# Optimization experiments

Hardware: AMD Instinct MI355X
Metric: run time of the kernel (lower is better)

The kernel has to match this reference:

```python
import jax, jax.numpy as jnp
import numpy as np

B, S, D = 2, 2048, 1024
H = 16
DK = D // H  # 64
THETA = 10000.0
CLAMP = 80.0


def setup_inputs() -> dict:
    key = jax.random.key(0)
    ks = jax.random.split(key, 5)
    scale = 1.0 / np.sqrt(D)
    return {
        "x": jax.random.normal(ks[0], (B, S, D), jnp.float32),
        "Wq": jax.random.normal(ks[1], (D, D), jnp.float32) * scale,
        "Wk": jax.random.normal(ks[2], (D, D), jnp.float32) * scale,
        "Wv": jax.random.normal(ks[3], (D, D), jnp.float32) * scale,
        "Wo": jax.random.normal(ks[4], (D, D), jnp.float32) * scale,
    }


def _rope(x):
    # x: (B, H, S, DK); rotate interleaved even/odd pairs
    pos = jnp.arange(S, dtype=jnp.float32)  # token_positions = arange
    inv_freq = 1.0 / (THETA ** (jnp.arange(0, DK, 2, dtype=jnp.float32) / DK))
    ang = pos[:, None] * inv_freq[None, :]  # (S, DK/2)
    cos, sin = jnp.cos(ang), jnp.sin(ang)
    x1, x2 = x[..., 0::2], x[..., 1::2]
    r1 = x1 * cos - x2 * sin
    r2 = x1 * sin + x2 * cos
    out = jnp.stack([r1, r2], axis=-1).reshape(x.shape)
    return out


def reference(x, Wq, Wk, Wv, Wo):
    # fused-style QKV projections (bias-free Linear: y = x @ W^T)
    def proj(W):
        y = jnp.einsum('bsd,ed->bse', x, W)
        return y.reshape(B, S, H, DK).transpose(0, 2, 1, 3)  # b h s dk
    Q, K, V = proj(Wq), proj(Wk), proj(Wv)
    Q, K = _rope(Q), _rope(K)
    # naive attention with score clamp then causal mask then scaled softmax
    scores = jnp.einsum('bhqd,bhkd->bhqk', Q, K)
    scores = jnp.clip(scores, -CLAMP, CLAMP)
    causal = jnp.tril(jnp.ones((S, S), dtype=bool))  # (q, k)
    scores = jnp.where(causal, scores, -jnp.inf)
    weights = jax.nn.softmax(scores / np.sqrt(DK), axis=-1)
    att = jnp.einsum('bhqk,bhkd->bhqd', weights, V)
    att = att.transpose(0, 2, 1, 3).reshape(B, S, D)
    return jnp.einsum('bsd,ed->bse', att, Wo)
```

## Files before the change

kernel.cpp:

```cpp
#include <hip/hip_runtime.h>
#include <hip/hip_bf16.h>

#define Bc 2
#define Sc 2048
#define Dc 1024
#define Hc 16
#define DKc 64
#define Mrows 4096

typedef __bf16 bf16;
typedef __bf16 bf16x8 __attribute__((ext_vector_type(8)));
typedef __bf16 bf16x4 __attribute__((ext_vector_type(4)));
typedef float f32x4 __attribute__((ext_vector_type(4)));

__global__ void cvt_f32_bf16(const float* __restrict__ in, bf16* __restrict__ out, int n) {
    int idx = (blockIdx.x * blockDim.x + threadIdx.x) * 4;
    if (idx < n) {
        float4 v = *(const float4*)(in + idx);
        bf16x4 o = { (bf16)v.x, (bf16)v.y, (bf16)v.z, (bf16)v.w };
        *(bf16x4*)(out + idx) = o;
    }
}

__global__ void cvt_w4(const float* __restrict__ a, const float* __restrict__ b,
                       const float* __restrict__ c, const float* __restrict__ d,
                       bf16* __restrict__ oa, bf16* __restrict__ ob,
                       bf16* __restrict__ oc, bf16* __restrict__ od) {
    int idx = (blockIdx.x * blockDim.x + threadIdx.x) * 4;
    const float* in; bf16* out;
    switch (blockIdx.y) {
        case 0: in = a; out = oa; break;
        case 1: in = b; out = ob; break;
        case 2: in = c; out = oc; break;
        default: in = d; out = od; break;
    }
    float4 v = *(const float4*)(in + idx);
    bf16x4 o = { (bf16)v.x, (bf16)v.y, (bf16)v.z, (bf16)v.w };
    *(bf16x4*)(out + idx) = o;
}

__device__ __forceinline__ void gld_lds16(const bf16* g, bf16* l) {
    __builtin_amdgcn_global_load_lds((const __attribute__((address_space(1))) void*)g,
                                     (__attribute__((address_space(3))) void*)l, 16, 0, 0);
}

template <typename OutT>
__global__ __launch_bounds__(512) void gemm_bt(const bf16* __restrict__ A,
                                               const bf16* __restrict__ Bt,
                                               OutT* __restrict__ C,
                                               int M, int N, int K) {
    __shared__ bf16 As[128 * 64];
    __shared__ bf16 Bs[128 * 64];
    const int tid = threadIdx.x;
    const int bm = blockIdx.y * 128, bn = blockIdx.x * 128;
    const int w = tid >> 6, l = tid & 63;
    const int wr = w >> 2, wc = w & 3;
    const int lr = l & 15, lc = l >> 4;

    const int srow = l >> 3;
    const int gl = (l & 7) ^ srow;
    const bf16* Ag = A  + (size_t)(bm + w * 16 + srow) * K + gl * 8;
    const bf16* Bg = Bt + (size_t)(bn + w * 16 + srow) * K + gl * 8;

    f32x4 acc[4][2] = {};

    for (int k0 = 0; k0 < K; k0 += 64) {
        __syncthreads();
#pragma unroll
        for (int c = 0; c < 2; c++) {
            gld_lds16(Ag + (size_t)(c * 8) * K + k0, &As[(w * 16 + c * 8) * 64]);
            gld_lds16(Bg + (size_t)(c * 8) * K + k0, &Bs[(w * 16 + c * 8) * 64]);
        }
        __syncthreads();
#pragma unroll
        for (int s = 0; s < 2; s++) {
            bf16x8 af[4], bfr[2];
#pragma unroll
            for (int i = 0; i < 4; i++) {
                const int R = wr * 64 + i * 16 + lr;
                af[i] = *(bf16x8*)&As[R * 64 + (((s * 4 + lc) ^ (R & 7)) * 8)];
            }
#pragma unroll
            for (int j = 0; j < 2; j++) {
                const int R = wc * 32 + j * 16 + lr;
                bfr[j] = *(bf16x8*)&Bs[R * 64 + (((s * 4 + lc) ^ (R & 7)) * 8)];
            }
#pragma unroll
            for (int i = 0; i < 4; i++)
#pragma unroll
                for (int j = 0; j < 2; j++)
                    acc[i][j] = __builtin_amdgcn_mfma_f32_16x16x32_bf16(af[i], bfr[j], acc[i][j], 0, 0, 0);
        }
    }

    const int cr = (l >> 4) * 4, cc = l & 15;
#pragma unroll
    for (int i = 0; i < 4; i++)
#pragma unroll
        for (int j = 0; j < 2; j++)
#pragma unroll
            for (int r = 0; r < 4; r++) {
                int row = bm + wr * 64 + i * 16 + cr + r;
                int col = bn + wc * 32 + j * 16 + cc;
                C[(size_t)row * N + col] = (OutT)acc[i][j][r];
            }
}

__global__ void rope_k(bf16* __restrict__ Q, bf16* __restrict__ K) {
    int i = blockIdx.x * blockDim.x + threadIdx.x;
    int pair = i & 31;
    int h = (i >> 5) & 15;
    int s = (i >> 9) & 2047;
    int b = i >> 20;
    float inv_freq = __powf(10000.0f, -((2.0f * pair) / 64.0f));
    float ang = (float)s * inv_freq;
    float c = cosf(ang), sn = sinf(ang);
    size_t base = ((size_t)(b * Sc + s)) * Dc + h * 64 + pair * 2;
    float q1 = (float)Q[base], q2 = (float)Q[base + 1];
    Q[base]     = (bf16)(q1 * c - q2 * sn);
    Q[base + 1] = (bf16)(q1 * sn + q2 * c);
    float k1 = (float)K[base], k2 = (float)K[base + 1];
    K[base]     = (bf16)(k1 * c - k2 * sn);
    K[base + 1] = (bf16)(k1 * sn + k2 * c);
}

#define LDA 72
__global__ __launch_bounds__(256) void attn_k(const bf16* __restrict__ Q,
                                              const bf16* __restrict__ Kt,
                                              const bf16* __restrict__ V,
                                              bf16* __restrict__ Oa) {
    __shared__ bf16 Ks[2][64 * LDA];
    __shared__ bf16 Vs[2][64 * LDA];
    __shared__ bf16 Ps[4][16 * LDA];

    const int bid = blockIdx.x;
    const int qi = 31 - (bid >> 5);
    const int bh = bid & 31;
    const int h = bh & 15, b = bh >> 4;
    const int q0 = qi * 64;
    const int tid = threadIdx.x, w = tid >> 6, l = tid & 63;
    const int lr = l & 15, lc = l >> 4;

    const bf16* Qb = Q  + ((size_t)b * Sc) * Dc + h * 64;
    const bf16* Kb = Kt + ((size_t)b * Sc) * Dc + h * 64;
    const bf16* Vb = V  + ((size_t)b * Sc) * Dc + h * 64;

    const int qrow = q0 + w * 16 + lr;
    bf16x8 qf0 = *(const bf16x8*)(Qb + (size_t)qrow * Dc + lc * 8);
    bf16x8 qf1 = *(const bf16x8*)(Qb + (size_t)qrow * Dc + 32 + lc * 8);

    f32x4 oacc[4] = {};
    float psum[4] = {0.f, 0.f, 0.f, 0.f};

    const int nt = qi + 1;
    const int skey = tid >> 3, sdk = (tid & 7) * 8;
    const int vkey = tid & 63, vdk0 = (tid >> 6) * 16;

    bf16x8 kr0, kr1, vr0, vr1;
#define LOADT(T) { const size_t kk = (size_t)(T) * 64;                          \
        kr0 = *(const bf16x8*)(Kb + (kk + skey) * Dc + sdk);                    \
        kr1 = *(const bf16x8*)(Kb + (kk + skey + 32) * Dc + sdk);               \
        vr0 = *(const bf16x8*)(Vb + (kk + vkey) * Dc + vdk0);                   \
        vr1 = *(const bf16x8*)(Vb + (kk + vkey) * Dc + vdk0 + 8); }
#define WRITET(BUF) {                                                           \
        *(bf16x8*)&Ks[BUF][skey * LDA + sdk] = kr0;                             \
        *(bf16x8*)&Ks[BUF][(skey + 32) * LDA + sdk] = kr1;                      \
        _Pragma("unroll") for (int e = 0; e < 8; e++) {                         \
            Vs[BUF][(vdk0 + e) * LDA + vkey] = vr0[e];                          \
            Vs[BUF][(vdk0 + 8 + e) * LDA + vkey] = vr1[e]; } }

    LOADT(0); WRITET(0);
    int cur = 0;
    for (int t = 0; t < nt; t++) {
        const int k0 = t * 64;
        if (t + 1 < nt) LOADT(t + 1);
        __syncthreads();

        f32x4 sfr[4];
#pragma unroll
        for (int j = 0; j < 4; j++) {
            bf16x8 b0 = *(bf16x8*)&Ks[cur][(j * 16 + lr) * LDA + lc * 8];
            bf16x8 b1 = *(bf16x8*)&Ks[cur][(j * 16 + lr) * LDA + 32 + lc * 8];
            f32x4 z = {};
            z = __builtin_amdgcn_mfma_f32_16x16x32_bf16(qf0, b0, z, 0, 0, 0);
            z = __builtin_amdgcn_mfma_f32_16x16x32_bf16(qf1, b1, z, 0, 0, 0);
            sfr[j] = z;
        }

        const bool diag = (t == nt - 1);
#pragma unroll
        for (int j = 0; j < 4; j++) {
            const int kg = k0 + j * 16 + lr;
#pragma unroll
            for (int r = 0; r < 4; r++) {
                float s = sfr[j][r];
                s = fminf(fmaxf(s, -80.0f), 80.0f) * 0.125f;
                float p = __expf(s - 10.0f);
                if (diag && kg > (q0 + w * 16 + lc * 4 + r)) p = 0.0f;
                psum[r] += p;
                Ps[w][(lc * 4 + r) * LDA + j * 16 + lr] = (bf16)p;
            }
        }

#pragma unroll
        for (int c = 0; c < 2; c++) {
            bf16x8 pf = *(bf16x8*)&Ps[w][lr * LDA + c * 32 + lc * 8];
#pragma unroll
            for (int j = 0; j < 4; j++) {
                bf16x8 vf = *(bf16x8*)&Vs[cur][(j * 16 + lr) * LDA + c * 32 + lc * 8];
                oacc[j] = __builtin_amdgcn_mfma_f32_16x16x32_bf16(pf, vf, oacc[j], 0, 0, 0);
            }
        }

        if (t + 1 < nt) WRITET(cur ^ 1);
        cur ^= 1;
    }

#pragma unroll
    for (int d = 1; d < 16; d <<= 1)
#pragma unroll
        for (int r = 0; r < 4; r++) psum[r] += __shfl_xor(psum[r], d, 64);

    bf16* Ob = Oa + ((size_t)b * Sc) * Dc + h * 64;
#pragma unroll
    for (int j = 0; j < 4; j++)
#pragma unroll
        for (int r = 0; r < 4; r++) {
            int qg = q0 + w * 16 + lc * 4 + r;
            Ob[(size_t)qg * Dc + j * 16 + lr] = (bf16)(oacc[j][r] / psum[r]);
        }
}

extern "C" void kernel_launch(void* const* d_in, const int* in_sizes, int n_in,
                              void* d_out, int out_size, void* d_ws, size_t ws_size,
                              hipStream_t stream) {
    const float* x  = (const float*)d_in[0];
    const float* Wq = (const float*)d_in[1];
    const float* Wk = (const float*)d_in[2];
    const float* Wv = (const float*)d_in[3];
    const float* Wo = (const float*)d_in[4];

    const int NX = Bc * Sc * Dc;
    const int NW = Dc * Dc;

    bf16* xb  = (bf16*)d_ws;
    bf16* wqb = xb + NX;
    bf16* wkb = wqb + NW;
    bf16* wvb = wkb + NW;
    bf16* wob = wvb + NW;
    bf16* Yq  = wob + NW;
    bf16* Yk  = Yq + NX;
    bf16* Yv  = Yk + NX;
    bf16* att = Yv + NX;

    cvt_f32_bf16<<<NX / 4 / 256, 256, 0, stream>>>(x, xb, NX);
    cvt_w4<<<dim3(NW / 4 / 256, 4), 256, 0, stream>>>(Wq, Wk, Wv, Wo, wqb, wkb, wvb, wob);

    dim3 gg(Dc / 128, Mrows / 128);
    gemm_bt<bf16><<<gg, 512, 0, stream>>>(xb, wqb, Yq, Mrows, Dc, Dc);
    gemm_bt<bf16><<<gg, 512, 0, stream>>>(xb, wkb, Yk, Mrows, Dc, Dc);
    gemm_bt<bf16><<<gg, 512, 0, stream>>>(xb, wvb, Yv, Mrows, Dc, Dc);

    rope_k<<<(Bc * Sc * Hc * 32) / 256, 256, 0, stream>>>(Yq, Yk);

    attn_k<<<Bc * Hc * (Sc / 64), 256, 0, stream>>>(Yq, Yk, Yv, att);

    gemm_bt<float><<<gg, 512, 0, stream>>>(att, wob, (float*)d_out, Mrows, Dc, Dc);
}
```

Measured before the change: 222.5 us.

## Fuse QKV GEMMs, pre-transpose V, and rework attention staging with async LDS loads

The three Q/K/V projections become one GEMM with N=3072. This relies on wqb, wkb and wvb sitting next to each other in the workspace, forming one stacked 3072x1024 weight. A separate kernel transposes V into a head-major layout. The attention kernel now stages K and V tiles with global_load_lds into XOR-swizzled shared memory, and passes P between lanes with ds_bpermute in registers instead of a shared-memory round trip. The intent is to cut launch count, LDS traffic and bank conflicts, at the cost of an extra transpose pass and tighter reliance on the workspace layout.

```diff
diff --git a/kernel.cpp b/kernel.cpp
--- a/kernel.cpp
+++ b/kernel.cpp
@@ -7,6 +7,7 @@
 #define Hc 16
 #define DKc 64
 #define Mrows 4096
+#define QKV_LD 3072
 
 typedef __bf16 bf16;
 typedef __bf16 bf16x8 __attribute__((ext_vector_type(8)));
@@ -42,6 +43,10 @@
 __device__ __forceinline__ void gld_lds16(const bf16* g, bf16* l) {
     __builtin_amdgcn_global_load_lds((const __attribute__((address_space(1))) void*)g,
                                      (__attribute__((address_space(3))) void*)l, 16, 0, 0);
+}
+
+__device__ __forceinline__ unsigned bperm(int addrBytes, unsigned v) {
+    return (unsigned)__builtin_amdgcn_ds_bpermute(addrBytes, (int)v);
 }
 
 template <typename OutT>
@@ -106,32 +111,59 @@
             }
 }
 
-__global__ void rope_k(bf16* __restrict__ Q, bf16* __restrict__ K) {
+__global__ void rope_k(bf16* __restrict__ QKV) {
     int i = blockIdx.x * blockDim.x + threadIdx.x;
     int pair = i & 31;
     int h = (i >> 5) & 15;
     int s = (i >> 9) & 2047;
     int b = i >> 20;
-    float inv_freq = __powf(10000.0f, -((2.0f * pair) / 64.0f));
+    float inv_freq = exp2f(-0.41524101186f * (float)pair);
     float ang = (float)s * inv_freq;
     float c = cosf(ang), sn = sinf(ang);
-    size_t base = ((size_t)(b * Sc + s)) * Dc + h * 64 + pair * 2;
-    float q1 = (float)Q[base], q2 = (float)Q[base + 1];
-    Q[base]     = (bf16)(q1 * c - q2 * sn);
-    Q[base + 1] = (bf16)(q1 * sn + q2 * c);
-    float k1 = (float)K[base], k2 = (float)K[base + 1];
-    K[base]     = (bf16)(k1 * c - k2 * sn);
-    K[base + 1] = (bf16)(k1 * sn + k2 * c);
-}
-
-#define LDA 72
-__global__ __launch_bounds__(256) void attn_k(const bf16* __restrict__ Q,
-                                              const bf16* __restrict__ Kt,
-                                              const bf16* __restrict__ V,
+    size_t base = ((size_t)(b * Sc + s)) * QKV_LD + h * 64 + pair * 2;
+    float q1 = (float)QKV[base], q2 = (float)QKV[base + 1];
+    QKV[base]     = (bf16)(q1 * c - q2 * sn);
+    QKV[base + 1] = (bf16)(q1 * sn + q2 * c);
+    size_t kb = base + 1024;
+    float k1 = (float)QKV[kb], k2 = (float)QKV[kb + 1];
+    QKV[kb]     = (bf16)(k1 * c - k2 * sn);
+    QKV[kb + 1] = (bf16)(k1 * sn + k2 * c);
+}
+
+__global__ __launch_bounds__(256) void vtrans(const bf16* __restrict__ QKV, bf16* __restrict__ Vt) {
+    __shared__ bf16 T[64 * 68];
+    const int s0 = blockIdx.x * 64;
+    const int bh = blockIdx.y;
+    const int b = bh >> 4, h = bh & 15;
+    const int tid = threadIdx.x;
+    const bf16* src = QKV + (size_t)(b * Sc + s0) * QKV_LD + 2048 + h * 64;
+#pragma unroll
+    for (int p = 0; p < 2; p++) {
+        int sr = (tid >> 3) + p * 32;
+        int dk0 = (tid & 7) * 8;
+        bf16x8 v = *(const bf16x8*)(src + (size_t)sr * QKV_LD + dk0);
+        bf16x4 lo = { v[0], v[1], v[2], v[3] }, hi = { v[4], v[5], v[6], v[7] };
+        *(bf16x4*)&T[sr * 68 + dk0]     = lo;
+        *(bf16x4*)&T[sr * 68 + dk0 + 4] = hi;
+    }
+    __syncthreads();
+    bf16* dst = Vt + (size_t)(bh * 64) * Sc + s0;
+#pragma unroll
+    for (int p = 0; p < 2; p++) {
+        int dk = (tid >> 3) + p * 32;
+        int sc0 = (tid & 7) * 8;
+        bf16x8 v;
+#pragma unroll
+        for (int e = 0; e < 8; e++) v[e] = T[(sc0 + e) * 68 + dk];
+        *(bf16x8*)(dst + (size_t)dk * Sc + sc0) = v;
+    }
+}
+
+__global__ __launch_bounds__(256) void attn_k(const bf16* __restrict__ QKV,
+                                              const bf16* __restrict__ Vt,
                                               bf16* __restrict__ Oa) {
-    __shared__ bf16 Ks[2][64 * LDA];
-    __shared__ bf16 Vs[2][64 * LDA];
-    __shared__ bf16 Ps[4][16 * LDA];
+    __shared__ bf16 Ks[2][64 * 64];
+    __shared__ bf16 Vs[2][64 * 64];
 
     const int bid = blockIdx.x;
     const int qi = 31 - (bid >> 5);
@@ -141,94 +173,123 @@
     const int tid = threadIdx.x, w = tid >> 6, l = tid & 63;
     const int lr = l & 15, lc = l >> 4;
 
-    const bf16* Qb = Q  + ((size_t)b * Sc) * Dc + h * 64;
-    const bf16* Kb = Kt + ((size_t)b * Sc) * Dc + h * 64;
-    const bf16* Vb = V  + ((size_t)b * Sc) * Dc + h * 64;
+    const bf16* Qb  = QKV + (size_t)(b * Sc) * QKV_LD + h * 64;
+    const bf16* Kb  = QKV + (size_t)(b * Sc) * QKV_LD + 1024 + h * 64;
+    const bf16* Vtb = Vt + (size_t)(bh * 64) * Sc;
 
     const int qrow = q0 + w * 16 + lr;
-    bf16x8 qf0 = *(const bf16x8*)(Qb + (size_t)qrow * Dc + lc * 8);
-    bf16x8 qf1 = *(const bf16x8*)(Qb + (size_t)qrow * Dc + 32 + lc * 8);
+    bf16x8 qf0 = *(const bf16x8*)(Qb + (size_t)qrow * QKV_LD + lc * 8);
+    bf16x8 qf1 = *(const bf16x8*)(Qb + (size_t)qrow * QKV_LD + 32 + lc * 8);
+
+    const int r8 = l >> 3, glg = (l & 7) ^ r8;
+    const bf16* Kg = Kb  + (size_t)(16 * w + r8) * QKV_LD + glg * 8;
+    const bf16* Vg = Vtb + (size_t)(16 * w + r8) * Sc + glg * 8;
 
     f32x4 oacc[4] = {};
-    float psum[4] = {0.f, 0.f, 0.f, 0.f};
+    float psum = 0.f;
+
+    const int sA = (lr + ((lc & 1) << 5)) << 2;
+    const int sB = sA + (16 << 2);
+    const bool hij = (lc & 2) != 0;
 
     const int nt = qi + 1;
-    const int skey = tid >> 3, sdk = (tid & 7) * 8;
-    const int vkey = tid & 63, vdk0 = (tid >> 6) * 16;
-
-    bf16x8 kr0, kr1, vr0, vr1;
-#define LOADT(T) { const size_t kk = (size_t)(T) * 64;                          \
-        kr0 = *(const bf16x8*)(Kb + (kk + skey) * Dc + sdk);                    \
-        kr1 = *(const bf16x8*)(Kb + (kk + skey + 32) * Dc + sdk);               \
-        vr0 = *(const bf16x8*)(Vb + (kk + vkey) * Dc + vdk0);                   \
-        vr1 = *(const bf16x8*)(Vb + (kk + vkey) * Dc + vdk0 + 8); }
-#define WRITET(BUF) {                                                           \
-        *(bf16x8*)&Ks[BUF][skey * LDA + sdk] = kr0;                             \
-        *(bf16x8*)&Ks[BUF][(skey + 32) * LDA + sdk] = kr1;                      \
-        _Pragma("unroll") for (int e = 0; e < 8; e++) {                         \
-            Vs[BUF][(vdk0 + e) * LDA + vkey] = vr0[e];                          \
-            Vs[BUF][(vdk0 + 8 + e) * LDA + vkey] = vr1[e]; } }
-
-    LOADT(0); WRITET(0);
     int cur = 0;
+
+#define STAGE(T, BUF) {                                                            \
+    const size_t kof = (size_t)((T) * 64) * QKV_LD;                                \
+    const size_t vof = (size_t)((T) * 64);                                         \
+    gld_lds16(Kg + kof,                    &Ks[BUF][(16 * w) * 64]);               \
+    gld_lds16(Kg + kof + (size_t)8 * QKV_LD, &Ks[BUF][(16 * w + 8) * 64]);         \
+    gld_lds16(Vg + vof,                    &Vs[BUF][(16 * w) * 64]);               \
+    gld_lds16(Vg + vof + (size_t)8 * Sc,   &Vs[BUF][(16 * w + 8) * 64]); }
+
+    STAGE(0, 0);
     for (int t = 0; t < nt; t++) {
         const int k0 = t * 64;
-        if (t + 1 < nt) LOADT(t + 1);
-        __syncthreads();
+        if (t + 1 < nt) {
+            __builtin_amdgcn_s_barrier();
+            STAGE(t + 1, cur ^ 1);
+            asm volatile("s_waitcnt vmcnt(4)" ::: "memory");
+        } else {
+            asm volatile("s_waitcnt vmcnt(0)" ::: "memory");
+        }
+        __builtin_amdgcn_s_barrier();
 
         f32x4 sfr[4];
 #pragma unroll
         for (int j = 0; j < 4; j++) {
-            bf16x8 b0 = *(bf16x8*)&Ks[cur][(j * 16 + lr) * LDA + lc * 8];
-            bf16x8 b1 = *(bf16x8*)&Ks[cur][(j * 16 + lr) * LDA + 32 + lc * 8];
+            const int R = j * 16 + lr;
+            bf16x8 kf0 = *(bf16x8*)&Ks[cur][R * 64 + ((lc ^ (lr & 7)) * 8)];
+            bf16x8 kf1 = *(bf16x8*)&Ks[cur][R * 64 + (((4 + lc) ^ (lr & 7)) * 8)];
             f32x4 z = {};
-            z = __builtin_amdgcn_mfma_f32_16x16x32_bf16(qf0, b0, z, 0, 0, 0);
-            z = __builtin_amdgcn_mfma_f32_16x16x32_bf16(qf1, b1, z, 0, 0, 0);
+            z = __builtin_amdgcn_mfma_f32_16x16x32_bf16(kf0, qf0, z, 0, 0, 0);
+            z = __builtin_amdgcn_mfma_f32_16x16x32_bf16(kf1, qf1, z, 0, 0, 0);
             sfr[j] = z;
         }
 
         const bool diag = (t == nt - 1);
+        const int qg = q0 + w * 16 + lr;
+        float pv[4][4];
+#pragma unroll
+        for (int j = 0; j < 4; j++)
+#pragma unroll
+            for (int r = 0; r < 4; r++) {
+                float s = fminf(fmaxf(sfr[j][r], -80.f), 80.f);
+                float p = __expf(s * 0.125f - 10.0f);
+                if (diag && (k0 + j * 16 + lc * 4 + r) > qg) p = 0.f;
+                psum += p;
+                pv[j][r] = p;
+            }
+
+        unsigned pw0[4], pw1[4];
 #pragma unroll
         for (int j = 0; j < 4; j++) {
-            const int kg = k0 + j * 16 + lr;
-#pragma unroll
-            for (int r = 0; r < 4; r++) {
-                float s = sfr[j][r];
-                s = fminf(fmaxf(s, -80.0f), 80.0f) * 0.125f;
-                float p = __expf(s - 10.0f);
-                if (diag && kg > (q0 + w * 16 + lc * 4 + r)) p = 0.0f;
-                psum[r] += p;
-                Ps[w][(lc * 4 + r) * LDA + j * 16 + lr] = (bf16)p;
-            }
-        }
-
-#pragma unroll
-        for (int c = 0; c < 2; c++) {
-            bf16x8 pf = *(bf16x8*)&Ps[w][lr * LDA + c * 32 + lc * 8];
-#pragma unroll
-            for (int j = 0; j < 4; j++) {
-                bf16x8 vf = *(bf16x8*)&Vs[cur][(j * 16 + lr) * LDA + c * 32 + lc * 8];
-                oacc[j] = __builtin_amdgcn_mfma_f32_16x16x32_bf16(pf, vf, oacc[j], 0, 0, 0);
-            }
-        }
-
-        if (t + 1 < nt) WRITET(cur ^ 1);
+            asm("v_cvt_pk_bf16_f32 %0, %1, %2" : "=v"(pw0[j]) : "v"(pv[j][0]), "v"(pv[j][1]));
+            asm("v_cvt_pk_bf16_f32 %0, %1, %2" : "=v"(pw1[j]) : "v"(pv[j][2]), "v"(pv[j][3]));
+        }
+
+        union { int4 i; bf16x8 h; } u0, u1;
+        {
+            unsigned t0 = bperm(sA, pw0[0]), s0_ = bperm(sA, pw0[1]);
+            unsigned t1 = bperm(sA, pw1[0]), s1_ = bperm(sA, pw1[1]);
+            unsigned t2 = bperm(sB, pw0[0]), s2_ = bperm(sB, pw0[1]);
+            unsigned t3 = bperm(sB, pw1[0]), s3_ = bperm(sB, pw1[1]);
+            u0.i = (int4){ (int)(hij ? s0_ : t0), (int)(hij ? s1_ : t1),
+                           (int)(hij ? s2_ : t2), (int)(hij ? s3_ : t3) };
+            unsigned v0 = bperm(sA, pw0[2]), r0_ = bperm(sA, pw0[3]);
+            unsigned v1 = bperm(sA, pw1[2]), r1_ = bperm(sA, pw1[3]);
+            unsigned v2 = bperm(sB, pw0[2]), r2_ = bperm(sB, pw0[3]);
+            unsigned v3 = bperm(sB, pw1[2]), r3_ = bperm(sB, pw1[3]);
+            u1.i = (int4){ (int)(hij ? r0_ : v0), (int)(hij ? r1_ : v1),
+                           (int)(hij ? r2_ : v2), (int)(hij ? r3_ : v3) };
+        }
+
+#pragma unroll
+        for (int jd = 0; jd < 4; jd++) {
+            const int R = jd * 16 + lr;
+            bf16x8 vf0 = *(bf16x8*)&Vs[cur][R * 64 + ((lc ^ (lr & 7)) * 8)];
+            bf16x8 vf1 = *(bf16x8*)&Vs[cur][R * 64 + (((4 + lc) ^ (lr & 7)) * 8)];
+            oacc[jd] = __builtin_amdgcn_mfma_f32_16x16x32_bf16(u0.h, vf0, oacc[jd], 0, 0, 0);
+            oacc[jd] = __builtin_amdgcn_mfma_f32_16x16x32_bf16(u1.h, vf1, oacc[jd], 0, 0, 0);
+        }
         cur ^= 1;
     }
 
-#pragma unroll
-    for (int d = 1; d < 16; d <<= 1)
-#pragma unroll
-        for (int r = 0; r < 4; r++) psum[r] += __shfl_xor(psum[r], d, 64);
-
-    bf16* Ob = Oa + ((size_t)b * Sc) * Dc + h * 64;
-#pragma unroll
-    for (int j = 0; j < 4; j++)
+    psum += __shfl_xor(psum, 16, 64);
+    psum += __shfl_xor(psum, 32, 64);
+    float pr[4];
+#pragma unroll
+    for (int r = 0; r < 4; r++) pr[r] = __shfl(psum, lc * 4 + r, 64);
+
+    bf16* Ob = Oa + (size_t)(b * Sc) * Dc + h * 64;
+#pragma unroll
+    for (int jd = 0; jd < 4; jd++)
 #pragma unroll
         for (int r = 0; r < 4; r++) {
-            int qg = q0 + w * 16 + lc * 4 + r;
-            Ob[(size_t)qg * Dc + j * 16 + lr] = (bf16)(oacc[j][r] / psum[r]);
-        }
+            int qg2 = q0 + w * 16 + lc * 4 + r;
+            Ob[(size_t)qg2 * Dc + jd * 16 + lr] = (bf16)(oacc[jd][r] / pr[r]);
+        }
+#undef STAGE
 }
 
 extern "C" void kernel_launch(void* const* d_in, const int* in_sizes, int n_in,
@@ -243,27 +304,24 @@
     const int NX = Bc * Sc * Dc;
     const int NW = Dc * Dc;
 
-    bf16* xb  = (bf16*)d_ws;
-    bf16* wqb = xb + NX;
-    bf16* wkb = wqb + NW;
-    bf16* wvb = wkb + NW;
-    bf16* wob = wvb + NW;
-    bf16* Yq  = wob + NW;
-    bf16* Yk  = Yq + NX;
-    bf16* Yv  = Yk + NX;
-    bf16* att = Yv + NX;
+    bf16* xb   = (bf16*)d_ws;
+    bf16* wqb  = xb + NX;
+    bf16* wkb  = wqb + NW;
+    bf16* wvb  = wkb + NW;
+    bf16* wob  = wvb + NW;
+    bf16* QKV  = wob + NW;
+    bf16* Vt   = QKV + (size_t)Mrows * QKV_LD;
+    bf16* att  = xb;
 
     cvt_f32_bf16<<<NX / 4 / 256, 256, 0, stream>>>(x, xb, NX);
     cvt_w4<<<dim3(NW / 4 / 256, 4), 256, 0, stream>>>(Wq, Wk, Wv, Wo, wqb, wkb, wvb, wob);
 
-    dim3 gg(Dc / 128, Mrows / 128);
-    gemm_bt<bf16><<<gg, 512, 0, stream>>>(xb, wqb, Yq, Mrows, Dc, Dc);
-    gemm_bt<bf16><<<gg, 512, 0, stream>>>(xb, wkb, Yk, Mrows, Dc, Dc);
-    gemm_bt<bf16><<<gg, 512, 0, stream>>>(xb, wvb, Yv, Mrows, Dc, Dc);
-
-    rope_k<<<(Bc * Sc * Hc * 32) / 256, 256, 0, stream>>>(Yq, Yk);
-
-    attn_k<<<Bc * Hc * (Sc / 64), 256, 0, stream>>>(Yq, Yk, Yv, att);
-
-    gemm_bt<float><<<gg, 512, 0, stream>>>(att, wob, (float*)d_out, Mrows, Dc, Dc);
-}
+    gemm_bt<bf16><<<dim3(QKV_LD / 128, Mrows / 128), 512, 0, stream>>>(xb, wqb, QKV, Mrows, QKV_LD, Dc);
+
+    rope_k<<<(Bc * Sc * Hc * 32) / 256, 256, 0, stream>>>(QKV);
+    vtrans<<<dim3(Sc / 64, Bc * Hc), 256, 0, stream>>>(QKV, Vt);
+
+    attn_k<<<Bc * Hc * (Sc / 64), 256, 0, stream>>>(QKV, Vt, att);
+
+    gemm_bt<float><<<dim3(Dc / 128, Mrows / 128), 512, 0, stream>>>(att, wob, (float*)d_out, Mrows, Dc, Dc);
+}
```

Measured after the change: 188.2 us. -15.4%, faster.
